# Optimization experiments

Hardware: AMD Instinct MI355X
Metric: run time of the kernel (lower is better)

The kernel has to match this reference:

```python
import jax, jax.numpy as jnp
import numpy as np

NSAMPLE = 64
RADIUS = 0.08
EPS = 1e-5
B, N, M, C = 4, 16384, 1024, 256


def ball_query(xyz, new_xyz, radius, nsample):
    """xyz [B,N,3], new_xyz [B,M,3] -> idx [B,M,nsample] int32.
    Picks first `nsample` points within `radius` of each query (in point order),
    padding with the first found index (0 if none), matching pointnet2 CUDA op."""
    b, n = xyz.shape[0], xyz.shape[1]
    m = new_xyz.shape[1]
    # squared distances via norms + matmul (avoids [B,M,N,3] intermediate)
    d2 = (jnp.sum(new_xyz * new_xyz, -1)[:, :, None]
          + jnp.sum(xyz * xyz, -1)[:, None, :]
          - 2.0 * jnp.einsum('bmc,bnc->bmn', new_xyz, xyz))  # [B,M,N]
    mask = d2 < radius * radius
    rank = jnp.cumsum(mask.astype(jnp.int32), axis=-1) - 1   # slot of each valid point
    valid = mask & (rank < nsample)
    slots = jnp.where(valid, rank, nsample)                  # invalid -> dump slot
    n_idx = jnp.broadcast_to(jnp.arange(n, dtype=jnp.int32), (b, m, n))
    b_idx = jnp.arange(b)[:, None, None]
    m_idx = jnp.arange(m)[None, :, None]
    idx = jnp.zeros((b, m, nsample + 1), jnp.int32)
    idx = idx.at[b_idx, m_idx, slots].set(n_idx)[..., :nsample]
    cnt = jnp.sum(mask, axis=-1)                             # [B,M] neighbors found
    pad = jnp.arange(nsample)[None, None, :] >= cnt[:, :, None]
    idx = jnp.where(pad, idx[:, :, :1], idx)                 # pad with first index
    return idx


def _mlp_layer(x, W, bias, gamma, beta, mu, var):
    # 1x1 conv (pointwise) + BatchNorm (eval, running stats) + ReLU, channels-last
    y = jnp.einsum('bmsc,oc->bmso', x, W) + bias
    y = (y - mu) * (gamma * jax.lax.rsqrt(var + EPS)) + beta
    return jax.nn.relu(y)


def reference(seed_xyz_fps, seed_xyz_graspable, seed_features_graspable,
              W1, b1, g1, be1, m1, v1, W2, b2, g2, be2, m2, v2):
    idx = ball_query(seed_xyz_fps, seed_xyz_graspable, RADIUS, NSAMPLE)  # [B,M,S]
    # gather + relative coordinates (use_xyz=True, normalize_xyz=False)
    gxyz = jax.vmap(lambda p, i: p[i])(seed_xyz_fps, idx)                # [B,M,S,3]
    gxyz = gxyz - seed_xyz_graspable[:, :, None, :]
    feats = jnp.swapaxes(seed_features_graspable, 1, 2)                  # [B,N,C]
    gfeat = jax.vmap(lambda f, i: f[i])(feats, idx)                      # [B,M,S,C]
    x = jnp.concatenate([gxyz, gfeat], axis=-1)                          # [B,M,S,3+C]
    x = _mlp_layer(x, W1, b1, g1, be1, m1, v1)                           # [B,M,S,256]
    x = _mlp_layer(x, W2, b2, g2, be2, m2, v2)                           # [B,M,S,256]
    x = jnp.max(x, axis=2)                                               # [B,M,256]
    return jnp.swapaxes(x, 1, 2)                                         # [B,256,M]


def setup_inputs() -> dict:
    key = jax.random.key(0)
    ks = jax.random.split(key, 16)
    return {
        'seed_xyz_fps': jax.random.uniform(ks[0], (B, N, 3), jnp.float32),
        'seed_xyz_graspable': jax.random.uniform(ks[1], (B, M, 3), jnp.float32),
        'seed_features_graspable': jax.random.normal(ks[2], (B, C, N), jnp.float32),
        'W1': jax.random.normal(ks[3], (256, 3 + C), jnp.float32) * 0.05,
        'b1': jax.random.normal(ks[4], (256,), jnp.float32) * 0.05,
        'g1': jax.random.uniform(ks[5], (256,), jnp.float32, 0.5, 1.5),
        'be1': jax.random.normal(ks[6], (256,), jnp.float32) * 0.05,
        'm1': jax.random.normal(ks[7], (256,), jnp.float32) * 0.1,
        'v1': jax.random.uniform(ks[8], (256,), jnp.float32, 0.5, 1.5),
        'W2': jax.random.normal(ks[9], (256, 256), jnp.float32) * 0.05,
        'b2': jax.random.normal(ks[10], (256,), jnp.float32) * 0.05,
        'g2': jax.random.uniform(ks[11], (256,), jnp.float32, 0.5, 1.5),
        'be2': jax.random.normal(ks[12], (256,), jnp.float32) * 0.05,
        'm2': jax.random.normal(ks[13], (256,), jnp.float32) * 0.1,
        'v2': jax.random.uniform(ks[14], (256,), jnp.float32, 0.5, 1.5),
    }
```

## Files before the change

### kernel.cpp

```cpp
#include <hip/hip_runtime.h>
#include <stdint.h>

typedef __bf16 bf16x8 __attribute__((ext_vector_type(8)));
typedef float f32x4 __attribute__((ext_vector_type(4)));

#define NSAMPLE 64
static constexpr int Bb = 4, Nn = 16384, Mm = 1024, Cc = 256;

__device__ __forceinline__ unsigned short f2bf(float f) {
  unsigned int u = __builtin_bit_cast(unsigned int, f);
  u = u + 0x7fffu + ((u >> 16) & 1u);
  return (unsigned short)(u >> 16);
}
__device__ __forceinline__ float bf2f(unsigned short u) {
  return __builtin_bit_cast(float, (unsigned int)u << 16);
}

__device__ __forceinline__ void gload_lds16(const void* g, void* lds) {
  __builtin_amdgcn_global_load_lds(
      (const __attribute__((address_space(1))) uint32_t*)g,
      (__attribute__((address_space(3))) uint32_t*)lds, 16, 0, 0);
}

__global__ void prep_kernel(const float* __restrict__ W1, const float* __restrict__ b1,
                            const float* __restrict__ g1, const float* __restrict__ be1,
                            const float* __restrict__ m1, const float* __restrict__ v1,
                            const float* __restrict__ W2, const float* __restrict__ b2,
                            const float* __restrict__ g2, const float* __restrict__ be2,
                            const float* __restrict__ m2, const float* __restrict__ v2,
                            unsigned short* __restrict__ W1b, float* __restrict__ w1c,
                            float* __restrict__ b1e,
                            unsigned short* __restrict__ W2b, float* __restrict__ b2e) {
  int t = blockIdx.x * 256 + threadIdx.x;
  {
    int o = t >> 8, k = t & 255;
    float s1 = g1[o] / sqrtf(v1[o] + 1e-5f);
    W1b[t] = f2bf(W1[o * 259 + 3 + k] * s1);
    float s2 = g2[o] / sqrtf(v2[o] + 1e-5f);
    W2b[t] = f2bf(W2[t] * s2);
  }
  if (t < 256 * 3) {
    int o = t / 3, c = t - o * 3;
    float s = g1[o] / sqrtf(v1[o] + 1e-5f);
    w1c[t] = W1[o * 259 + c] * s;
  }
  if (t < 256) {
    float s1 = g1[t] / sqrtf(v1[t] + 1e-5f);
    b1e[t] = s1 * (b1[t] - m1[t]) + be1[t];
    float s2 = g2[t] / sqrtf(v2[t] + 1e-5f);
    b2e[t] = s2 * (b2[t] - m2[t]) + be2[t];
  }
}

__global__ __launch_bounds__(256) void ballq_x1all_kernel(
    const float* __restrict__ xyz, const float* __restrict__ new_xyz,
    const float* __restrict__ feats, const unsigned short* __restrict__ W1b,
    unsigned short* __restrict__ X1all, int* __restrict__ idx) {
  __shared__ __align__(16) char smem[16640 + 32768];
  int bx = blockIdx.x;
  int t = threadIdx.x;
  if (bx < 1024) {
    int* wl = (int*)smem;
    int* wcnt = (int*)(smem + 4096);
    const float r2 = (float)(0.08 * 0.08);
    int bm0 = bx * 4;
    int lane = t & 63, w = t >> 6;
    int b = bm0 >> 10;
    float qx[4], qy[4], qz[4], qq[4];
    int cnt[4];
#pragma unroll
    for (int qi = 0; qi < 4; qi++) {
      qx[qi] = new_xyz[(bm0 + qi) * 3];
      qy[qi] = new_xyz[(bm0 + qi) * 3 + 1];
      qz[qi] = new_xyz[(bm0 + qi) * 3 + 2];
      qq[qi] = __fadd_rn(__fadd_rn(__fmul_rn(qx[qi], qx[qi]), __fmul_rn(qy[qi], qy[qi])),
                         __fmul_rn(qz[qi], qz[qi]));
      cnt[qi] = 0;
    }
    const float* P = xyz + ((size_t)b * Nn + w * 4096) * 3;
    for (int n0 = 0; n0 < 4096; n0 += 64) {
      const float* pp = P + (n0 + lane) * 3;
      float x = pp[0], y = pp[1], z = pp[2];
      float p2 = __fadd_rn(__fadd_rn(__fmul_rn(x, x), __fmul_rn(y, y)), __fmul_rn(z, z));
#pragma unroll
      for (int qi = 0; qi < 4; qi++) {
        if (cnt[qi] >= NSAMPLE) continue;
        float dt = __fadd_rn(__fadd_rn(__fmul_rn(qx[qi], x), __fmul_rn(qy[qi], y)),
                             __fmul_rn(qz[qi], z));
        float d2 = __fsub_rn(__fadd_rn(qq[qi], p2), __fmul_rn(2.f, dt));
        bool valid = d2 < r2;
        unsigned long long mask = __ballot(valid);
        if (mask) {
          if (valid) {
            int pos = cnt[qi] + __popcll(mask & ((1ull << lane) - 1ull));
            if (pos < NSAMPLE) wl[(qi * 4 + w) * 64 + pos] = w * 4096 + n0 + lane;
          }
          cnt[qi] += (int)__popcll(mask);
        }
      }
      if (cnt[0] >= NSAMPLE && cnt[1] >= NSAMPLE && cnt[2] >= NSAMPLE && cnt[3] >= NSAMPLE)
        break;
    }
    if (lane == 0) {
#pragma unroll
      for (int qi = 0; qi < 4; qi++) wcnt[qi * 4 + w] = cnt[qi];
    }
    __syncthreads();
    {
      int qi = t >> 6, s = t & 63;
      int c0 = wcnt[qi * 4], c1 = wcnt[qi * 4 + 1], c2 = wcnt[qi * 4 + 2], c3 = wcnt[qi * 4 + 3];
      int tot = c0 + c1 + c2 + c3;
      int cc = tot < NSAMPLE ? tot : NSAMPLE;
      int v;
      if (s < cc) {
        if (s < c0) v = wl[(qi * 4 + 0) * 64 + s];
        else if (s < c0 + c1) v = wl[(qi * 4 + 1) * 64 + s - c0];
        else if (s < c0 + c1 + c2) v = wl[(qi * 4 + 2) * 64 + s - c0 - c1];
        else v = wl[(qi * 4 + 3) * 64 + s - c0 - c1 - c2];
      } else {
        v = (c0 > 0) ? wl[(qi * 4 + 0) * 64] : (c1 > 0) ? wl[(qi * 4 + 1) * 64]
          : (c2 > 0) ? wl[(qi * 4 + 2) * 64] : (c3 > 0) ? wl[(qi * 4 + 3) * 64] : 0;
      }
      idx[(size_t)(bm0 + qi) * NSAMPLE + s] = v;
    }
    return;
  }
  float(*ftile)[65] = (float(*)[65])smem;
  unsigned short* Xf = (unsigned short*)(smem + 16640);
  int xb = bx - 1024;
  int b = xb >> 8, nt = xb & 255, n0 = nt * 64;
  for (int ct = 0; ct < 4; ct++) {
    const float* src = feats + ((size_t)(b * Cc + ct * 64)) * Nn + n0;
    int tx = t & 63, ty = t >> 6;
#pragma unroll
    for (int i = 0; i < 16; i++) {
      int c = i * 4 + ty;
      ftile[c][tx] = src[(size_t)c * Nn + tx];
    }
    __syncthreads();
    int c4 = (t & 15) * 4, nr = t >> 4;
#pragma unroll
    for (int i = 0; i < 4; i++) {
      int n = i * 16 + nr;
      int cg = ct * 8 + (c4 >> 3);
      int sc = cg ^ (n & 7);
      ushort4 v;
      v.x = f2bf(ftile[c4][n]);
      v.y = f2bf(ftile[c4 + 1][n]);
      v.z = f2bf(ftile[c4 + 2][n]);
      v.w = f2bf(ftile[c4 + 3][n]);
      *(ushort4*)&Xf[n * 256 + sc * 8 + (c4 & 7)] = v;
    }
    __syncthreads();
  }
  int wave = t >> 6, lane = t & 63;
  int lr = lane & 15, kg = lane >> 4;
  int wcol = wave * 64;
  f32x4 acc[4][4];
#pragma unroll
  for (int mi = 0; mi < 4; mi++)
#pragma unroll
    for (int ni = 0; ni < 4; ni++) acc[mi][ni] = (f32x4){0.f, 0.f, 0.f, 0.f};
#pragma unroll
  for (int kk = 0; kk < 8; kk++) {
    bf16x8 w[4];
#pragma unroll
    for (int ni = 0; ni < 4; ni++)
      w[ni] = *(const bf16x8*)&W1b[(size_t)(wcol + ni * 16 + lr) * 256 + kk * 32 + kg * 8];
    bf16x8 a[4];
#pragma unroll
    for (int mi = 0; mi < 4; mi++) {
      int r = mi * 16 + lr;
      int cs = ((kk * 4 + kg) ^ (r & 7)) * 8;
      a[mi] = *(const bf16x8*)&Xf[r * 256 + cs];
    }
#pragma unroll
    for (int mi = 0; mi < 4; mi++)
#pragma unroll
      for (int ni = 0; ni < 4; ni++)
        acc[mi][ni] = __builtin_amdgcn_mfma_f32_16x16x32_bf16(a[mi], w[ni], acc[mi][ni], 0, 0, 0);
  }
  __syncthreads();
#pragma unroll
  for (int ni = 0; ni < 4; ni++) {
    int o = wcol + ni * 16 + lr;
#pragma unroll
    for (int mi = 0; mi < 4; mi++)
#pragma unroll
      for (int j = 0; j < 4; j++) {
        int r = mi * 16 + kg * 4 + j;
        Xf[r * 256 + o] = f2bf(acc[mi][ni][j]);
      }
  }
  __syncthreads();
  {
    int row = t >> 2, off = (t & 3) * 64;
    unsigned short* dst = X1all + ((size_t)(b * Nn + n0 + row)) * 256 + off;
#pragma unroll
    for (int i = 0; i < 8; i++)
      *(uint4*)(dst + i * 8) = *(const uint4*)&Xf[row * 256 + off + i * 8];
  }
}

__global__ __launch_bounds__(256, 4) void fused_kernel(
    const unsigned short* __restrict__ X1all, const float* __restrict__ xyz,
    const float* __restrict__ new_xyz, const int* __restrict__ idx,
    const float* __restrict__ w1c, const float* __restrict__ b1e,
    const unsigned short* __restrict__ W2b, const float* __restrict__ b2e,
    float* __restrict__ out) {
  __shared__ unsigned short Xf[64 * 256];
  __shared__ float Xc[3][64];
  __shared__ float Cw[4][256];
  int t = threadIdx.x;
  int wave = t >> 6, lane = t & 63;
  int lr = lane & 15, kg = lane >> 4;
  int wcol = wave * 64;
  int bm = blockIdx.x;
  int b = bm >> 10;

  {
    int idxr = idx[(size_t)bm * NSAMPLE + wave * 16 + (lane & 15)];
#pragma unroll
    for (int i = 0; i < 8; i++) {
      int j = wave * 8 + i;
      int iv = __shfl(idxr, 2 * i + (lane >> 5));
      int r7 = (2 * j + (lane >> 5)) & 7;
      int cg = (lane & 31) ^ r7;
      gload_lds16(X1all + ((size_t)b * Nn + iv) * Cc + cg * 8, &Xf[j * 512]);
    }
  }
  if (t < 64) {
    int ci = idx[(size_t)bm * NSAMPLE + t];
    const float* pp = xyz + ((size_t)b * Nn + ci) * 3;
    Xc[0][t] = pp[0] - new_xyz[bm * 3];
    Xc[1][t] = pp[1] - new_xyz[bm * 3 + 1];
    Xc[2][t] = pp[2] - new_xyz[bm * 3 + 2];
  }
  {
    Cw[0][t] = b1e[t];
    Cw[1][t] = w1c[t * 3];
    Cw[2][t] = w1c[t * 3 + 1];
    Cw[3][t] = w1c[t * 3 + 2];
  }
  __syncthreads();

  {
    int s = t >> 2, c0 = (t & 3) * 64;
    float cx = Xc[0][s], cy = Xc[1][s], cz = Xc[2][s];
#pragma unroll
    for (int g = 0; g < 8; g++) {
      int cg = (c0 >> 3) + g;
      int sc = cg ^ (s & 7);
      unsigned short* p = &Xf[s * 256 + sc * 8];
      uint4 v = *(uint4*)p;
      unsigned short* e = (unsigned short*)&v;
#pragma unroll
      for (int j = 0; j < 8; j++) {
        int o = cg * 8 + j;
        float h = bf2f(e[j]) + Cw[0][o] + cx * Cw[1][o] + cy * Cw[2][o] + cz * Cw[3][o];
        e[j] = f2bf(fmaxf(h, 0.f));
      }
      *(uint4*)p = v;
    }
  }
  __syncthreads();

  f32x4 acc[4][4];
#pragma unroll
  for (int mi = 0; mi < 4; mi++)
#pragma unroll
    for (int ni = 0; ni < 4; ni++) acc[mi][ni] = (f32x4){0.f, 0.f, 0.f, 0.f};
#pragma unroll
  for (int kk = 0; kk < 8; kk++) {
    bf16x8 w[4];
#pragma unroll
    for (int ni = 0; ni < 4; ni++)
      w[ni] = *(const bf16x8*)&W2b[(size_t)(wcol + ni * 16 + lr) * 256 + kk * 32 + kg * 8];
    bf16x8 a[4];
#pragma unroll
    for (int mi = 0; mi < 4; mi++) {
      int r = mi * 16 + lr;
      int cs = ((kk * 4 + kg) ^ (r & 7)) * 8;
      a[mi] = *(const bf16x8*)&Xf[r * 256 + cs];
    }
#pragma unroll
    for (int mi = 0; mi < 4; mi++)
#pragma unroll
      for (int ni = 0; ni < 4; ni++)
        acc[mi][ni] = __builtin_amdgcn_mfma_f32_16x16x32_bf16(a[mi], w[ni], acc[mi][ni], 0, 0, 0);
  }
  {
    int m = bm & (Mm - 1);
#pragma unroll
    for (int ni = 0; ni < 4; ni++) {
      float bv = b2e[wcol + ni * 16 + lr];
      float v = 0.f;
#pragma unroll
      for (int mi = 0; mi < 4; mi++)
#pragma unroll
        for (int j = 0; j < 4; j++) v = fmaxf(v, acc[mi][ni][j] + bv);
      v = fmaxf(v, __shfl_xor(v, 16));
      v = fmaxf(v, __shfl_xor(v, 32));
      if (kg == 0)
        out[((size_t)b * 256 + wcol + ni * 16 + lr) * Mm + m] = v;
    }
  }
}

extern "C" void kernel_launch(void* const* d_in, const int* in_sizes, int n_in,
                              void* d_out, int out_size, void* d_ws, size_t ws_size,
                              hipStream_t stream) {
  (void)in_sizes; (void)n_in; (void)out_size; (void)ws_size;
  const float* xyz     = (const float*)d_in[0];
  const float* new_xyz = (const float*)d_in[1];
  const float* feats   = (const float*)d_in[2];
  const float* W1 = (const float*)d_in[3];
  const float* b1 = (const float*)d_in[4];
  const float* g1 = (const float*)d_in[5];
  const float* be1 = (const float*)d_in[6];
  const float* m1 = (const float*)d_in[7];
  const float* v1 = (const float*)d_in[8];
  const float* W2 = (const float*)d_in[9];
  const float* b2 = (const float*)d_in[10];
  const float* g2 = (const float*)d_in[11];
  const float* be2 = (const float*)d_in[12];
  const float* m2 = (const float*)d_in[13];
  const float* v2 = (const float*)d_in[14];
  float* out = (float*)d_out;

  char* ws = (char*)d_ws;
  unsigned short* W1b   = (unsigned short*)(ws + 0);
  unsigned short* W2b   = (unsigned short*)(ws + 131072);
  float*          w1c   = (float*)(ws + 262144);
  float*          b1e   = (float*)(ws + 265216);
  float*          b2e   = (float*)(ws + 266240);
  unsigned short* X1all = (unsigned short*)(ws + 267264);
  int*            idx   = (int*)(ws + 33821696);

  prep_kernel<<<256, 256, 0, stream>>>(
      W1, b1, g1, be1, m1, v1, W2, b2, g2, be2, m2, v2, W1b, w1c, b1e, W2b, b2e);
  ballq_x1all_kernel<<<1024 + 1024, 256, 0, stream>>>(xyz, new_xyz, feats, W1b, X1all, idx);
  fused_kernel<<<Bb * Mm, 256, 0, stream>>>(X1all, xyz, new_xyz, idx,
                                            w1c, b1e, W2b, b2e, out);
}
```

Measured before the change: 169.3 us.

## Shrink X1 GEMM tile to 32 points, transpose features directly, remap bias/ReLU pass

The feature-projection blocks now handle 32 points instead of 64. Each thread reads 8 channels straight from global memory and writes swizzled bf16 into LDS, which removes the fp32 transpose tile and its extra barriers. The smaller LDS footprint and a launch bound of 4 blocks are meant to raise occupancy and double the block count. In fused_kernel, the bias/xyz/ReLU epilogue is reorganised so each thread keeps per-channel constants in registers across four rows instead of reloading them from LDS. The trade-off is that W1b fragments are re-read per 32-point tile, doubling global weight traffic, and the direct strided feature loads may coalesce less well.

Measured after the change: 146.6 us. 1.15x faster.

```diff
diff --git a/kernel.cpp b/kernel.cpp
--- a/kernel.cpp
+++ b/kernel.cpp
@@ -52,16 +52,16 @@
   }
 }
 
-__global__ __launch_bounds__(256) void ballq_x1all_kernel(
+__global__ __launch_bounds__(256, 4) void k2_kernel(
     const float* __restrict__ xyz, const float* __restrict__ new_xyz,
     const float* __restrict__ feats, const unsigned short* __restrict__ W1b,
     unsigned short* __restrict__ X1all, int* __restrict__ idx) {
-  __shared__ __align__(16) char smem[16640 + 32768];
+  __shared__ __align__(16) char smem[16384 + 64];
   int bx = blockIdx.x;
   int t = threadIdx.x;
   if (bx < 1024) {
     int* wl = (int*)smem;
-    int* wcnt = (int*)(smem + 4096);
+    int* wcnt = (int*)(smem + 16384);
     const float r2 = (float)(0.08 * 0.08);
     int bm0 = bx * 4;
     int lane = t & 63, w = t >> 6;
@@ -125,40 +125,30 @@
     }
     return;
   }
-  float(*ftile)[65] = (float(*)[65])smem;
-  unsigned short* Xf = (unsigned short*)(smem + 16640);
+  unsigned short* Xf = (unsigned short*)smem;
   int xb = bx - 1024;
-  int b = xb >> 8, nt = xb & 255, n0 = nt * 64;
-  for (int ct = 0; ct < 4; ct++) {
-    const float* src = feats + ((size_t)(b * Cc + ct * 64)) * Nn + n0;
-    int tx = t & 63, ty = t >> 6;
-#pragma unroll
-    for (int i = 0; i < 16; i++) {
-      int c = i * 4 + ty;
-      ftile[c][tx] = src[(size_t)c * Nn + tx];
-    }
-    __syncthreads();
-    int c4 = (t & 15) * 4, nr = t >> 4;
-#pragma unroll
-    for (int i = 0; i < 4; i++) {
-      int n = i * 16 + nr;
-      int cg = ct * 8 + (c4 >> 3);
-      int sc = cg ^ (n & 7);
-      ushort4 v;
-      v.x = f2bf(ftile[c4][n]);
-      v.y = f2bf(ftile[c4 + 1][n]);
-      v.z = f2bf(ftile[c4 + 2][n]);
-      v.w = f2bf(ftile[c4 + 3][n]);
-      *(ushort4*)&Xf[n * 256 + sc * 8 + (c4 & 7)] = v;
-    }
-    __syncthreads();
-  }
+  int b = xb >> 9, nt = xb & 511, n0 = nt * 32;
+  {
+    int nloc = t & 31, cgrp = t >> 5;
+    const float* src = feats + ((size_t)(b * Cc + cgrp * 32)) * Nn + n0 + nloc;
+#pragma unroll
+    for (int q = 0; q < 4; q++) {
+      unsigned short e[8];
+#pragma unroll
+      for (int j = 0; j < 8; j++)
+        e[j] = f2bf(src[(size_t)(q * 8 + j) * Nn]);
+      int cg = cgrp * 4 + q;
+      int sc = cg ^ (nloc & 7);
+      *(uint4*)&Xf[nloc * 256 + sc * 8] = *(uint4*)e;
+    }
+  }
+  __syncthreads();
   int wave = t >> 6, lane = t & 63;
   int lr = lane & 15, kg = lane >> 4;
   int wcol = wave * 64;
-  f32x4 acc[4][4];
-#pragma unroll
-  for (int mi = 0; mi < 4; mi++)
+  f32x4 acc[2][4];
+#pragma unroll
+  for (int mi = 0; mi < 2; mi++)
 #pragma unroll
     for (int ni = 0; ni < 4; ni++) acc[mi][ni] = (f32x4){0.f, 0.f, 0.f, 0.f};
 #pragma unroll
@@ -167,15 +157,15 @@
 #pragma unroll
     for (int ni = 0; ni < 4; ni++)
       w[ni] = *(const bf16x8*)&W1b[(size_t)(wcol + ni * 16 + lr) * 256 + kk * 32 + kg * 8];
-    bf16x8 a[4];
-#pragma unroll
-    for (int mi = 0; mi < 4; mi++) {
+    bf16x8 a[2];
+#pragma unroll
+    for (int mi = 0; mi < 2; mi++) {
       int r = mi * 16 + lr;
       int cs = ((kk * 4 + kg) ^ (r & 7)) * 8;
       a[mi] = *(const bf16x8*)&Xf[r * 256 + cs];
     }
 #pragma unroll
-    for (int mi = 0; mi < 4; mi++)
+    for (int mi = 0; mi < 2; mi++)
 #pragma unroll
       for (int ni = 0; ni < 4; ni++)
         acc[mi][ni] = __builtin_amdgcn_mfma_f32_16x16x32_bf16(a[mi], w[ni], acc[mi][ni], 0, 0, 0);
@@ -185,7 +175,7 @@
   for (int ni = 0; ni < 4; ni++) {
     int o = wcol + ni * 16 + lr;
 #pragma unroll
-    for (int mi = 0; mi < 4; mi++)
+    for (int mi = 0; mi < 2; mi++)
 #pragma unroll
       for (int j = 0; j < 4; j++) {
         int r = mi * 16 + kg * 4 + j;
@@ -194,10 +184,10 @@
   }
   __syncthreads();
   {
-    int row = t >> 2, off = (t & 3) * 64;
+    int row = t >> 3, off = (t & 7) * 32;
     unsigned short* dst = X1all + ((size_t)(b * Nn + n0 + row)) * 256 + off;
 #pragma unroll
-    for (int i = 0; i < 8; i++)
+    for (int i = 0; i < 4; i++)
       *(uint4*)(dst + i * 8) = *(const uint4*)&Xf[row * 256 + off + i * 8];
   }
 }
@@ -244,20 +234,28 @@
   }
   __syncthreads();
 
-  {
-    int s = t >> 2, c0 = (t & 3) * 64;
-    float cx = Xc[0][s], cy = Xc[1][s], cz = Xc[2][s];
-#pragma unroll
-    for (int g = 0; g < 8; g++) {
-      int cg = (c0 >> 3) + g;
-      int sc = cg ^ (s & 7);
-      unsigned short* p = &Xf[s * 256 + sc * 8];
+#pragma unroll
+  for (int cc2 = 0; cc2 < 2; cc2++) {
+    int ch = (wave * 2 + cc2) * 4 + kg;
+    int o0 = ch * 8;
+    float b0[8], wx[8], wy[8], wz[8];
+#pragma unroll
+    for (int j = 0; j < 8; j++) {
+      b0[j] = Cw[0][o0 + j];
+      wx[j] = Cw[1][o0 + j];
+      wy[j] = Cw[2][o0 + j];
+      wz[j] = Cw[3][o0 + j];
+    }
+#pragma unroll
+    for (int mi = 0; mi < 4; mi++) {
+      int r = mi * 16 + lr;
+      float cx = Xc[0][r], cy = Xc[1][r], cz = Xc[2][r];
+      unsigned short* p = &Xf[r * 256 + (ch ^ (r & 7)) * 8];
       uint4 v = *(uint4*)p;
       unsigned short* e = (unsigned short*)&v;
 #pragma unroll
       for (int j = 0; j < 8; j++) {
-        int o = cg * 8 + j;
-        float h = bf2f(e[j]) + Cw[0][o] + cx * Cw[1][o] + cy * Cw[2][o] + cz * Cw[3][o];
+        float h = bf2f(e[j]) + b0[j] + cx * wx[j] + cy * wy[j] + cz * wz[j];
         e[j] = f2bf(fmaxf(h, 0.f));
       }
       *(uint4*)p = v;
@@ -339,7 +337,7 @@
 
   prep_kernel<<<256, 256, 0, stream>>>(
       W1, b1, g1, be1, m1, v1, W2, b2, g2, be2, m2, v2, W1b, w1c, b1e, W2b, b2e);
-  ballq_x1all_kernel<<<1024 + 1024, 256, 0, stream>>>(xyz, new_xyz, feats, W1b, X1all, idx);
+  k2_kernel<<<1024 + 2048, 256, 0, stream>>>(xyz, new_xyz, feats, W1b, X1all, idx);
   fused_kernel<<<Bb * Mm, 256, 0, stream>>>(X1all, xyz, new_xyz, idx,
                                             w1c, b1e, W2b, b2e, out);
 }
```
